# Optimization experiments

Measured on AMD Instinct MI355X. Metric: run time of the kernel, lower is better.

Reference implementation:

```python
import jax, jax.numpy as jnp
import numpy as np
from jax.scipy.linalg import block_diag

N_STATE, N_INPUT, HORIZON = 32, 16, 64


def setup_inputs() -> dict:
    key = jax.random.key(0)
    kA, kB, kC, kx = jax.random.split(key, 4)
    n_all = N_STATE + N_INPUT
    A = jax.random.normal(kA, (N_STATE, N_STATE), dtype=jnp.float32)
    B = jax.random.normal(kB, (N_STATE, N_INPUT), dtype=jnp.float32)
    Craw = jax.random.normal(kC, (HORIZON, n_all, n_all), dtype=jnp.float32)
    # symmetric positive-definite stage costs -> nonsingular KKT system
    C = jnp.einsum('tij,tkj->tik', Craw, Craw) / jnp.sqrt(jnp.float32(n_all)) \
        + jnp.eye(n_all, dtype=jnp.float32)
    x0 = jax.random.normal(kx, (N_STATE,), dtype=jnp.float32)
    return {"A": A, "B": B, "C": C, "T": HORIZON, "x0": x0}


def reference(A, B, C, T, x0):
    n_state = A.shape[0]
    n_input = B.shape[1]
    n_all = n_state + n_input
    dt = A.dtype

    # cost_mat: block-diagonal [n_all*T, n_all*T]
    cost_mat = block_diag(*C)

    # dynamics: [n_state*T, n_all*T]
    AB = jnp.concatenate((A, B), axis=1)              # [n_state, n_all]
    AB_blk = block_diag(*([AB] * (T - 1)))            # [(T-1)*n_state, (T-1)*n_all]
    dynamics = jnp.zeros((n_state * T, n_all * T), dtype=dt)
    dynamics = dynamics.at[:n_state, :n_state].set(jnp.eye(n_state, dtype=dt))
    dynamics = dynamics.at[n_state:n_state + (T - 1) * n_state,
                           :(T - 1) * n_all].set(AB_blk)
    # -I coupling entries: row n_state*t + i, col n_all*t + i, t=1..T-1
    t = jnp.arange(1, T)
    rows = (n_state * t)[:, None] + jnp.arange(n_state)[None, :]
    cols = (n_all * t)[:, None] + jnp.arange(n_state)[None, :]
    dynamics = dynamics.at[rows, cols].set(jnp.asarray(-1.0, dt))

    zero_mat = jnp.zeros((n_state * T, n_state * T), dtype=dt)
    full_mat = jnp.block([[cost_mat, dynamics.T],
                          [dynamics, zero_mat]])      # [(n_all+n_state)*T]^2

    # rhs: zeros except x0 at the start of the dynamics block
    sol = jnp.zeros(n_all * T + n_state * T, dtype=dt)
    sol = sol.at[n_all * T: n_all * T + n_state].set(x0)

    tau_mu = jnp.linalg.solve(full_mat, sol[:, None])[:, 0]
    tau_star = tau_mu[:n_all * T]
    mu_star = tau_mu[n_all * T:]
    return tau_star, mu_star
```

## Files before the change

### kernel.cpp

```cpp
#include <hip/hip_runtime.h>


namespace {

constexpr int NS  = 32;
constexpr int NI  = 16;
constexpr int NA  = 48;
constexpr int TT  = 64;
constexpr int NTH = 256;
constexpr int NBLK = 64;

using ull = unsigned long long;

__device__ __forceinline__ void fma4(float4& a, float s, const float4& b) {
  a.x += s * b.x; a.y += s * b.y; a.z += s * b.z; a.w += s * b.w;
}
__device__ __forceinline__ void fms4(float4& a, float s, const float4& b) {
  a.x -= s * b.x; a.y -= s * b.y; a.z -= s * b.z; a.w -= s * b.w;
}
__device__ __forceinline__ float dot4(const float4& a, const float4& b) {
  return a.x * b.x + a.y * b.y + a.z * b.z + a.w * b.w;
}
__device__ __forceinline__ float rdlane(float v, int l) {
  return __int_as_float(__builtin_amdgcn_readlane(__float_as_int(v), l));
}

__device__ __forceinline__ ull ald(const ull* p) {
  return __hip_atomic_load(p, __ATOMIC_RELAXED, __HIP_MEMORY_SCOPE_AGENT);
}
__device__ __forceinline__ void ast(ull* p, ull v) {
  __hip_atomic_store(p, v, __ATOMIC_RELAXED, __HIP_MEMORY_SCOPE_AGENT);
}
__device__ __forceinline__ float aldf(const float* p) {
  return __uint_as_float(__hip_atomic_load((const unsigned*)p,
      __ATOMIC_RELAXED, __HIP_MEMORY_SCOPE_AGENT));
}
__device__ __forceinline__ void astf(float* p, float v) {
  __hip_atomic_store((unsigned*)p, __float_as_uint(v),
      __ATOMIC_RELAXED, __HIP_MEMORY_SCOPE_AGENT);
}
__device__ __forceinline__ ull pack2(float x, float y) {
  return (ull)__float_as_uint(x) | ((ull)__float_as_uint(y) << 32);
}
__device__ __forceinline__ float2 unpack2(ull v) {
  return make_float2(__uint_as_float((unsigned)v),
                     __uint_as_float((unsigned)(v >> 32)));
}
__device__ __forceinline__ float4 ald4(const ull* p) {
  ull lo = ald(p), hi = ald(p + 1);
  float2 a = unpack2(lo), b = unpack2(hi);
  return make_float4(a.x, a.y, b.x, b.y);
}
__device__ __forceinline__ void ast4(ull* p, const float4& v) {
  ast(p, pack2(v.x, v.y)); ast(p + 1, pack2(v.z, v.w));
}

__device__ __forceinline__ unsigned fld(const unsigned* f) {
  return __hip_atomic_load(f, __ATOMIC_RELAXED, __HIP_MEMORY_SCOPE_AGENT);
}
__device__ __forceinline__ void fst(unsigned* f) {
  __hip_atomic_store(f, 1u, __ATOMIC_RELAXED, __HIP_MEMORY_SCOPE_AGENT);
}
__device__ __forceinline__ void waitf(const unsigned* f) {
  if (threadIdx.x == 0)
    while (fld(f) == 0) __builtin_amdgcn_s_sleep(1);
  __syncthreads();
}
__device__ __forceinline__ void setf(unsigned* f) {
  asm volatile("s_waitcnt vmcnt(0)" ::: "memory");
  __syncthreads();
  if (threadIdx.x == 0) fst(f);
}

template<int K>
__device__ __forceinline__ void tile_outer(const float* Acol0, int lda,
                                           const float* Bcol0, int ldb,
                                           float4 acc[4]) {
  #pragma unroll
  for (int m = 0; m < K; ++m) {
    const float4 va = *(const float4*)(Acol0 + m * lda);
    const float4 vb = *(const float4*)(Bcol0 + m * ldb);
    fma4(acc[0], va.x, vb); fma4(acc[1], va.y, vb);
    fma4(acc[2], va.z, vb); fma4(acc[3], va.w, vb);
  }
}

template<int KQ>
__device__ __forceinline__ void tile_dot(const float* Arow0, int lda,
                                         const float* Brow0, int ldb,
                                         float acc[4][4]) {
  #pragma unroll
  for (int q = 0; q < KQ; ++q) {
    float4 va[4], vb[4];
    #pragma unroll
    for (int r = 0; r < 4; ++r) va[r] = *(const float4*)(Arow0 + r * lda + 4 * q);
    #pragma unroll
    for (int c = 0; c < 4; ++c) vb[c] = *(const float4*)(Brow0 + c * ldb + 4 * q);
    #pragma unroll
    for (int r = 0; r < 4; ++r)
      #pragma unroll
      for (int c = 0; c < 4; ++c) acc[r][c] += dot4(va[r], vb[c]);
  }
}

__device__ __forceinline__ float step_dot(const float4 m[8], float x) {
  float a0 = 0.f, a1 = 0.f, a2 = 0.f, a3 = 0.f;
  #pragma unroll
  for (int q = 0; q < 8; ++q) {
    a0 += rdlane(x, 4 * q + 0) * m[q].x;
    a1 += rdlane(x, 4 * q + 1) * m[q].y;
    a2 += rdlane(x, 4 * q + 2) * m[q].z;
    a3 += rdlane(x, 4 * q + 3) * m[q].w;
  }
  return (a0 + a1) + (a2 + a3);
}

__device__ __forceinline__ int nlev(int rm) {
  return (rm == TT - 1) ? 0 : (32 - __clz(TT - 1 - rm));
}

__global__ __launch_bounds__(NTH, 1) void lqr_all(
    const float* __restrict__ A, const float* __restrict__ Bm,
    const float* __restrict__ C, const float* __restrict__ x0,
    float* __restrict__ out,
    float* __restrict__ Sb0, float* __restrict__ Sb1,
    float* __restrict__ Mall, float* __restrict__ xs,
    unsigned* __restrict__ flg) {
  __shared__ float sC [NA][NA];
  __shared__ float sAB[NS][NA];
  __shared__ float sRiST[NS][NI];
  __shared__ float sBRi [NS][NI];
  __shared__ float sAi[NS][NS], sCi[NS][NS], sJi[NS][NS];
  __shared__ float sAj[NS][NS], sCj[NS][NS], sJj[NS][NS], sAjT[NS][NS];
  __shared__ float sV[NS][NS], sU[NS][NS];
  __shared__ float sY1[NS][NS], sY2[NS][NS], sW[NS][NS];
  __shared__ float sX[NS][NS], sZm[NS][NS];
  __shared__ float sG[NS][NA], sFu[NI][NA], sK[NI][NS], sK2[NI][NS];
  __shared__ float sXt0[NS], sXt1[NS];

  const int t = blockIdx.x, tid = threadIdx.x, lane = tid & 63, wid = tid >> 6;
  unsigned* wr = flg;
  unsigned* rd = flg + 448;
  unsigned* mf = flg + 832;
  unsigned* xf = flg + 896;

  {
    const float* Ct = C + (size_t)t * NA * NA;
    for (int e = tid; e < NA * NA; e += NTH) sC[e / NA][e % NA] = Ct[e];
    for (int e = tid; e < NS * NA; e += NTH) {
      int i = e / NA, j = e % NA;
      sAB[i][j] = (j < NS) ? A[i * NS + j] : Bm[i * NI + (j - NS)];
    }
    __syncthreads();
    if (wid < 2 && lane < 48) {
      const int c = lane;
      float f[NI];
      if (c < NI) {
        #pragma unroll
        for (int i = 0; i < NI; ++i) f[i] = sC[NS + i][NS + c];
      } else {
        const int a = c - NI;
        if (wid == 0) {
          #pragma unroll
          for (int i = 0; i < NI; ++i) f[i] = sC[a][NS + i];
        } else {
          #pragma unroll
          for (int i = 0; i < NI; ++i) f[i] = sAB[a][NS + i];
        }
      }
      #pragma unroll
      for (int k = 0; k < NI; ++k) {
        float mi[NI];
        #pragma unroll
        for (int i = 0; i < NI; ++i) mi[i] = rdlane(f[i], k);
        const float inv = 1.0f / mi[k];
        f[k] *= inv;
        #pragma unroll
        for (int i = 0; i < NI; ++i) if (i != k) f[i] -= mi[i] * f[k];
      }
      if (c >= NI) {
        const int a = c - NI;
        float* D = (wid == 0) ? &sRiST[a][0] : &sBRi[a][0];
        #pragma unroll
        for (int i = 0; i < NI; ++i) D[i] = f[i];
      }
    }
    __syncthreads();
    ull* outA = (ull*)(Sb0 + (size_t)t * 3072);
    ull* outC = outA + 512;
    ull* outJ = outA + 1024;
    if (tid < 64) {
      const int a = tid >> 3, b = tid & 7;
      float acc[4][4];
      #pragma unroll
      for (int r = 0; r < 4; ++r)
        #pragma unroll
        for (int c = 0; c < 4; ++c) acc[r][c] = 0.f;
      tile_dot<4>(&sRiST[4 * a][0], NI, &sC[4 * b][NS], NA, acc);
      #pragma unroll
      for (int r = 0; r < 4; ++r) {
        const float4 q4 = *(const float4*)&sC[4 * a + r][4 * b];
        const float4 v = make_float4(q4.x - acc[r][0], q4.y - acc[r][1],
                                     q4.z - acc[r][2], q4.w - acc[r][3]);
        *(float4*)&sJi[4 * a + r][4 * b] = v;
        ast4(outJ + ((4 * a + r) * NS + 4 * b) / 2, v);
      }
    } else if (tid < 128) {
      const int q = tid - 64, a = q >> 3, b = q & 7;
      float acc[4][4];
      #pragma unroll
      for (int r = 0; r < 4; ++r)
        #pragma unroll
        for (int c = 0; c < 4; ++c) acc[r][c] = 0.f;
      tile_dot<4>(&sBRi[4 * a][0], NI, &sC[4 * b][NS], NA, acc);
      #pragma unroll
      for (int r = 0; r < 4; ++r) {
        const float4 a4 = *(const float4*)&sAB[4 * a + r][4 * b];
        const float4 v = make_float4(a4.x - acc[r][0], a4.y - acc[r][1],
                                     a4.z - acc[r][2], a4.w - acc[r][3]);
        *(float4*)&sAi[4 * a + r][4 * b] = v;
        ast4(outA + ((4 * a + r) * NS + 4 * b) / 2, v);
      }
    } else if (tid < 192) {
      const int q = tid - 128, a = q >> 3, b = q & 7;
      float acc[4][4];
      #pragma unroll
      for (int r = 0; r < 4; ++r)
        #pragma unroll
        for (int c = 0; c < 4; ++c) acc[r][c] = 0.f;
      tile_dot<4>(&sBRi[4 * a][0], NI, &sAB[4 * b][NS], NA, acc);
      #pragma unroll
      for (int r = 0; r < 4; ++r) {
        const float4 v = make_float4(acc[r][0], acc[r][1], acc[r][2], acc[r][3]);
        *(float4*)&sCi[4 * a + r][4 * b] = v;
        ast4(outC + ((4 * a + r) * NS + 4 * b) / 2, v);
      }
    }
  }
  setf(&wr[0 * 64 + t]);

  auto combine = [&]() {
    #pragma unroll
    for (int r = 0; r < 4; ++r) {
      const int e = tid + 256 * r, i = e >> 5, j = e & 31;
      sAjT[j][i] = sAj[i][j];
    }
    if (tid < 64) {
      const int a = tid >> 3, b = tid & 7;
      float4 acc[4] = {make_float4(0,0,0,0), make_float4(0,0,0,0),
                       make_float4(0,0,0,0), make_float4(0,0,0,0)};
      tile_outer<NS>(&sCi[0][4 * a], NS, &sJj[0][4 * b], NS, acc);
      if (a == b) { acc[0].x += 1.f; acc[1].y += 1.f; acc[2].z += 1.f; acc[3].w += 1.f; }
      #pragma unroll
      for (int r = 0; r < 4; ++r) *(float4*)&sX[4 * a + r][4 * b] = acc[r];
    }
    __syncthreads();
    if (wid < 2) {
      const int c = lane;
      float f[NS];
      if (c < NS) {
        #pragma unroll
        for (int i = 0; i < NS; ++i) f[i] = sX[i][c];
      } else if (wid == 0) {
        #pragma unroll
        for (int i = 0; i < NS; ++i) f[i] = sAi[i][c - NS];
      } else {
        #pragma unroll
        for (int i = 0; i < NS; ++i) f[i] = sCi[i][c - NS];
      }
      #pragma unroll
      for (int k = 0; k < NS; ++k) {
        float mi[NS];
        #pragma unroll
        for (int i = 0; i < NS; ++i) mi[i] = rdlane(f[i], k);
        const float inv = 1.0f / mi[k];
        f[k] *= inv;
        #pragma unroll
        for (int i = 0; i < NS; ++i) if (i != k) f[i] -= mi[i] * f[k];
      }
      if (c >= NS) {
        const int col = c - NS;
        if (wid == 0) {
          #pragma unroll
          for (int i = 0; i < NS; ++i) sV[i][col] = f[i];
        } else {
          #pragma unroll
          for (int i = 0; i < NS; ++i) sU[i][col] = f[i];
        }
      }
    }
    __syncthreads();
    if (tid < 192) {
      const int grp = tid >> 6, q = tid & 63, a = q >> 3, b = q & 7;
      float4 acc[4] = {make_float4(0,0,0,0), make_float4(0,0,0,0),
                       make_float4(0,0,0,0), make_float4(0,0,0,0)};
      if (grp == 0) {
        tile_outer<NS>(&sJj[0][4 * a], NS, &sV[0][4 * b], NS, acc);
        #pragma unroll
        for (int r = 0; r < 4; ++r) *(float4*)&sW[4 * a + r][4 * b] = acc[r];
      } else if (grp == 1) {
        tile_outer<NS>(&sAjT[0][4 * a], NS, &sV[0][4 * b], NS, acc);
        #pragma unroll
        for (int r = 0; r < 4; ++r) *(float4*)&sX[4 * a + r][4 * b] = acc[r];
      } else {
        tile_outer<NS>(&sAjT[0][4 * a], NS, &sU[0][4 * b], NS, acc);
        #pragma unroll
        for (int r = 0; r < 4; ++r) *(float4*)&sZm[4 * a + r][4 * b] = acc[r];
      }
    }
    __syncthreads();
    if (tid < 64) {
      const int a = tid >> 3, b = tid & 7;
      float4 acc[4] = {make_float4(0,0,0,0), make_float4(0,0,0,0),
                       make_float4(0,0,0,0), make_float4(0,0,0,0)};
      tile_outer<NS>(&sAi[0][4 * a], NS, &sW[0][4 * b], NS, acc);
      #pragma unroll
      for (int r = 0; r < 4; ++r) {
        const float4 j4 = *(const float4*)&sJi[4 * a + r][4 * b];
        acc[r].x += j4.x; acc[r].y += j4.y; acc[r].z += j4.z; acc[r].w += j4.w;
        *(float4*)&sY1[4 * a + r][4 * b] = acc[r];
      }
    } else if (tid < 128) {
      const int q = tid - 64, a = q >> 3, b = q & 7;
      float acc[4][4];
      #pragma unroll
      for (int r = 0; r < 4; ++r)
        #pragma unroll
        for (int c = 0; c < 4; ++c) acc[r][c] = 0.f;
      tile_dot<8>(&sZm[4 * a][0], NS, &sAj[4 * b][0], NS, acc);
      #pragma unroll
      for (int r = 0; r < 4; ++r) {
        const float4 c4 = *(const float4*)&sCj[4 * a + r][4 * b];
        *(float4*)&sY2[4 * a + r][4 * b] =
            make_float4(acc[r][0] + c4.x, acc[r][1] + c4.y,
                        acc[r][2] + c4.z, acc[r][3] + c4.w);
      }
    }
    __syncthreads();
    ((ull*)sAi)[tid] = ((const ull*)sX)[tid];
    ((ull*)sAi)[tid + 256] = ((const ull*)sX)[tid + 256];
    ((ull*)sCi)[tid] = ((const ull*)sY2)[tid];
    ((ull*)sCi)[tid + 256] = ((const ull*)sY2)[tid + 256];
    ((ull*)sJi)[tid] = ((const ull*)sY1)[tid];
    ((ull*)sJi)[tid + 256] = ((const ull*)sY1)[tid + 256];
    __syncthreads();
  };

  for (int l = 0; l < 6; ++l) {
    const int off = 1 << l;
    const int rm = t + off;
    if (rm < TT) {
      const int nlv = nlev(rm);
      const int v = (l < nlv) ? l : nlv;
      const float* Sin = (v & 1) ? Sb1 : Sb0;
      float* Sout = ((l + 1) & 1) ? Sb1 : Sb0;
      ull* Eo = (ull*)(Sout + (size_t)t * 3072);
      waitf(&wr[v * 64 + rm]);
      const ull* Ej = (const ull*)(Sin + (size_t)rm * 3072);
      {
        ull r0 = ald(Ej + tid),        r1 = ald(Ej + 256 + tid);
        ull r2 = ald(Ej + 512 + tid),  r3 = ald(Ej + 768 + tid);
        ull r4 = ald(Ej + 1024 + tid), r5 = ald(Ej + 1280 + tid);
        ((ull*)sAj)[tid] = r0; ((ull*)sAj)[tid + 256] = r1;
        ((ull*)sCj)[tid] = r2; ((ull*)sCj)[tid + 256] = r3;
        ((ull*)sJj)[tid] = r4; ((ull*)sJj)[tid + 256] = r5;
      }
      __syncthreads();
      if (v == l && tid == 0) fst(&rd[l * 64 + rm]);
      combine();
      if (l >= 1 && t >= (off >> 1)) waitf(&rd[(l - 1) * 64 + t]);
      ast(Eo + tid,        ((const ull*)sAi)[tid]);
      ast(Eo + 256 + tid,  ((const ull*)sAi)[tid + 256]);
      ast(Eo + 512 + tid,  ((const ull*)sCi)[tid]);
      ast(Eo + 768 + tid,  ((const ull*)sCi)[tid + 256]);
      ast(Eo + 1024 + tid, ((const ull*)sJi)[tid]);
      ast(Eo + 1280 + tid, ((const ull*)sJi)[tid + 256]);
      setf(&wr[(l + 1) * 64 + t]);
    }
  }

  auto kmat = [&](int tau, bool hasP, float (*Pm)[NS], float (*Kd)[NS], bool wM) {
    const int ui = tid / 12, uk = tid - 12 * ui;
    float4 cr0 = make_float4(0,0,0,0), cr1 = make_float4(0,0,0,0);
    float4 cr2 = make_float4(0,0,0,0), cr3 = make_float4(0,0,0,0);
    if (tid < 48) {
      const float* Ct = C + (size_t)tau * NA * NA;
      cr0 = *(const float4*)&Ct[(NS + 4 * ui + 0) * NA + 4 * uk];
      cr1 = *(const float4*)&Ct[(NS + 4 * ui + 1) * NA + 4 * uk];
      cr2 = *(const float4*)&Ct[(NS + 4 * ui + 2) * NA + 4 * uk];
      cr3 = *(const float4*)&Ct[(NS + 4 * ui + 3) * NA + 4 * uk];
    }
    if (hasP) {
      if (tid < 96) {
        const int gi = tid / 12, gk = tid - 12 * gi;
        float4 acc[4] = {make_float4(0,0,0,0), make_float4(0,0,0,0),
                         make_float4(0,0,0,0), make_float4(0,0,0,0)};
        tile_outer<NS>(&Pm[0][4 * gi], NS, &sAB[0][4 * gk], NA, acc);
        #pragma unroll
        for (int r = 0; r < 4; ++r) *(float4*)&sG[4 * gi + r][4 * gk] = acc[r];
      }
    } else {
      for (int e = tid; e < NS * NA; e += NTH) sG[e / NA][e % NA] = 0.f;
    }
    __syncthreads();
    if (tid < 48) {
      float4 acc[4] = {cr0, cr1, cr2, cr3};
      tile_outer<NS>(&sAB[0][NS + 4 * ui], NA, &sG[0][4 * uk], NA, acc);
      #pragma unroll
      for (int r = 0; r < 4; ++r) *(float4*)&sFu[4 * ui + r][4 * uk] = acc[r];
    }
    __syncthreads();
    if (wid == 0) {
      const int col = (lane < 16) ? (NS + lane) : (lane - 16);
      float f[NI];
      #pragma unroll
      for (int i = 0; i < NI; ++i) f[i] = sFu[i][col];
      #pragma unroll
      for (int k = 0; k < NI; ++k) {
        float mi[NI];
        #pragma unroll
        for (int i = 0; i < NI; ++i) mi[i] = rdlane(f[i], k);
        const float inv = 1.0f / mi[k];
        f[k] *= inv;
        #pragma unroll
        for (int i = 0; i < NI; ++i) if (i != k) f[i] -= mi[i] * f[k];
      }
      if (lane >= 16 && lane < 48) {
        const int b = lane - 16;
        #pragma unroll
        for (int i = 0; i < NI; ++i) Kd[i][b] = f[i];
      }
    }
    __syncthreads();
    if (wM && tid < 64) {
      const int ma = tid >> 3, mb = tid & 7;
      float4 a0 = *(const float4*)&sAB[4 * ma + 0][4 * mb];
      float4 a1 = *(const float4*)&sAB[4 * ma + 1][4 * mb];
      float4 a2 = *(const float4*)&sAB[4 * ma + 2][4 * mb];
      float4 a3 = *(const float4*)&sAB[4 * ma + 3][4 * mb];
      #pragma unroll
      for (int q = 0; q < 4; ++q) {
        const float4 vf0 = *(const float4*)&sAB[4 * ma + 0][NS + 4 * q];
        const float4 vf1 = *(const float4*)&sAB[4 * ma + 1][NS + 4 * q];
        const float4 vf2 = *(const float4*)&sAB[4 * ma + 2][NS + 4 * q];
        const float4 vf3 = *(const float4*)&sAB[4 * ma + 3][NS + 4 * q];
        #pragma unroll
        for (int d = 0; d < 4; ++d) {
          const float4 vkk = *(const float4*)&Kd[4 * q + d][4 * mb];
          const float s0 = (d == 0) ? vf0.x : (d == 1) ? vf0.y : (d == 2) ? vf0.z : vf0.w;
          const float s1 = (d == 0) ? vf1.x : (d == 1) ? vf1.y : (d == 2) ? vf1.z : vf1.w;
          const float s2 = (d == 0) ? vf2.x : (d == 1) ? vf2.y : (d == 2) ? vf2.z : vf2.w;
          const float s3 = (d == 0) ? vf3.x : (d == 1) ? vf3.y : (d == 2) ? vf3.z : vf3.w;
          fms4(a0, s0, vkk); fms4(a1, s1, vkk); fms4(a2, s2, vkk); fms4(a3, s3, vkk);
        }
      }
      ull* Mt = (ull*)(Mall + (size_t)tau * NS * NS);
      ast4(Mt + (4 * ma + 0) * 16 + 2 * mb, a0);
      ast4(Mt + (4 * ma + 1) * 16 + 2 * mb, a1);
      ast4(Mt + (4 * ma + 2) * 16 + 2 * mb, a2);
      ast4(Mt + (4 * ma + 3) * 16 + 2 * mb, a3);
    }
    __syncthreads();
  };

  if (t >= 1) kmat(t - 1, true, sJi, sK, true);
  if (t == TT - 1) kmat(TT - 1, false, nullptr, sK2, false);
  setf(&mf[t]);

  if (t == 0) {
    if (tid < NBLK) {
      while (fld(&mf[tid]) == 0) __builtin_amdgcn_s_sleep(1);
    }
    __syncthreads();
    if (wid == 0) {
      const int i = lane;
      if (i < NS) {
        const ull* Mg = (const ull*)Mall;
        float4 mA[8], mB[8];
        float x = x0[i];
        out[i] = x; astf(&xs[i], x);
        #pragma unroll
        for (int q = 0; q < 8; ++q) mA[q] = ald4(Mg + 0 * 512 + i * 16 + 2 * q);
        #pragma unroll
        for (int q = 0; q < 8; ++q) mB[q] = ald4(Mg + 1 * 512 + i * 16 + 2 * q);
        for (int s = 0; s < TT - 1; s += 2) {
          x = step_dot(mA, x);
          out[(s + 1) * NA + i] = x; astf(&xs[(s + 1) * NS + i], x);
          if (s + 2 < TT - 1) {
            #pragma unroll
            for (int q = 0; q < 8; ++q) mA[q] = ald4(Mg + (s + 2) * 512 + i * 16 + 2 * q);
          }
          if (s + 1 < TT - 1) {
            x = step_dot(mB, x);
            out[(s + 2) * NA + i] = x; astf(&xs[(s + 2) * NS + i], x);
            if (s + 3 < TT - 1) {
              #pragma unroll
              for (int q = 0; q < 8; ++q) mB[q] = ald4(Mg + (s + 3) * 512 + i * 16 + 2 * q);
            }
          }
        }
      }
    }
    setf(xf);
  }
  waitf(xf);

  {
    if (tid < NS) sXt0[tid] = aldf(&xs[(size_t)t * NS + tid]);
    else if (tid >= 64 && tid < 64 + NS && t >= 1)
      sXt1[tid - 64] = aldf(&xs[(size_t)(t - 1) * NS + (tid - 64)]);
    __syncthreads();
    if (t >= 1 && tid < NI) {
      const float4* Kr = (const float4*)&sK[tid][0];
      const float4* xr = (const float4*)sXt1;
      float acc = 0.f;
      #pragma unroll
      for (int q = 0; q < 8; ++q) acc += dot4(Kr[q], xr[q]);
      out[(t - 1) * NA + NS + tid] = -acc;
    } else if (tid >= NI && tid < NI + NS) {
      const int i = tid - NI;
      const float4* Pr = (const float4*)&sJi[i][0];
      const float4* xr = (const float4*)sXt0;
      float acc = 0.f;
      #pragma unroll
      for (int q = 0; q < 8; ++q) acc += dot4(Pr[q], xr[q]);
      out[NA * TT + t * NS + i] = (t == 0) ? -acc : acc;
    } else if (t == TT - 1 && tid >= 192 && tid < 192 + NI) {
      const int i = tid - 192;
      const float4* Kr = (const float4*)&sK2[i][0];
      const float4* xr = (const float4*)sXt0;
      float acc = 0.f;
      #pragma unroll
      for (int q = 0; q < 8; ++q) acc += dot4(Kr[q], xr[q]);
      out[(TT - 1) * NA + NS + i] = -acc;
    }
  }
}

}

extern "C" void kernel_launch(void* const* d_in, const int* in_sizes, int n_in,
                              void* d_out, int out_size, void* d_ws, size_t ws_size,
                              hipStream_t stream) {
  const float* A  = (const float*)d_in[0];
  const float* Bm = (const float*)d_in[1];
  const float* C  = (const float*)d_in[2];
  const float* x0 = (const float*)d_in[4];
  float* out = (float*)d_out;

  float* Sb0 = (float*)d_ws;
  float* Sb1 = Sb0 + (size_t)TT * 3072;
  float* Mall = Sb1 + (size_t)TT * 3072;
  float* xs   = Mall + (size_t)TT * NS * NS;
  unsigned* flg = (unsigned*)(xs + (size_t)TT * NS);

  hipMemsetAsync(flg, 0, 4096, stream);
  hipLaunchKernelGGL(lqr_all, dim3(NBLK), dim3(NTH), 0, stream,
                     A, Bm, C, x0, out, Sb0, Sb1, Mall, xs, flg);
}
```

Measured before the change: 143.3 us.

## Compute forward state rollout redundantly per block instead of broadcasting from block 0

Each block now waits on all M flags and runs the forward recurrence itself up to its own stage t, keeping x_t and x_{t-1} in shared memory. This removes the xs global buffer, block 0's serial broadcast and the xf flag wait, trading a cross-block handoff for redundant serial work (up to 63 steps in the last block). It also remaps blockIdx to t with a bit-swizzle, likely to spread stages across XCDs, and pads sAjT rows to 36 to reduce LDS bank conflicts.

New measurement: 126.6 us. 11.6% less time.

```diff
diff --git a/kernel.cpp b/kernel.cpp
--- a/kernel.cpp
+++ b/kernel.cpp
@@ -30,14 +30,6 @@
 }
 __device__ __forceinline__ void ast(ull* p, ull v) {
   __hip_atomic_store(p, v, __ATOMIC_RELAXED, __HIP_MEMORY_SCOPE_AGENT);
-}
-__device__ __forceinline__ float aldf(const float* p) {
-  return __uint_as_float(__hip_atomic_load((const unsigned*)p,
-      __ATOMIC_RELAXED, __HIP_MEMORY_SCOPE_AGENT));
-}
-__device__ __forceinline__ void astf(float* p, float v) {
-  __hip_atomic_store((unsigned*)p, __float_as_uint(v),
-      __ATOMIC_RELAXED, __HIP_MEMORY_SCOPE_AGENT);
 }
 __device__ __forceinline__ ull pack2(float x, float y) {
   return (ull)__float_as_uint(x) | ((ull)__float_as_uint(y) << 32);
@@ -124,25 +116,25 @@
     const float* __restrict__ C, const float* __restrict__ x0,
     float* __restrict__ out,
     float* __restrict__ Sb0, float* __restrict__ Sb1,
-    float* __restrict__ Mall, float* __restrict__ xs,
-    unsigned* __restrict__ flg) {
+    float* __restrict__ Mall, unsigned* __restrict__ flg) {
   __shared__ float sC [NA][NA];
   __shared__ float sAB[NS][NA];
   __shared__ float sRiST[NS][NI];
   __shared__ float sBRi [NS][NI];
   __shared__ float sAi[NS][NS], sCi[NS][NS], sJi[NS][NS];
-  __shared__ float sAj[NS][NS], sCj[NS][NS], sJj[NS][NS], sAjT[NS][NS];
+  __shared__ float sAj[NS][NS], sCj[NS][NS], sJj[NS][NS];
+  __shared__ float sAjT[NS][36];
   __shared__ float sV[NS][NS], sU[NS][NS];
   __shared__ float sY1[NS][NS], sY2[NS][NS], sW[NS][NS];
   __shared__ float sX[NS][NS], sZm[NS][NS];
   __shared__ float sG[NS][NA], sFu[NI][NA], sK[NI][NS], sK2[NI][NS];
   __shared__ float sXt0[NS], sXt1[NS];
 
-  const int t = blockIdx.x, tid = threadIdx.x, lane = tid & 63, wid = tid >> 6;
+  const int t = ((blockIdx.x & 7) << 3) | (blockIdx.x >> 3);
+  const int tid = threadIdx.x, lane = tid & 63, wid = tid >> 6;
   unsigned* wr = flg;
   unsigned* rd = flg + 448;
   unsigned* mf = flg + 832;
-  unsigned* xf = flg + 896;
 
   {
     const float* Ct = C + (size_t)t * NA * NA;
@@ -299,11 +291,11 @@
         #pragma unroll
         for (int r = 0; r < 4; ++r) *(float4*)&sW[4 * a + r][4 * b] = acc[r];
       } else if (grp == 1) {
-        tile_outer<NS>(&sAjT[0][4 * a], NS, &sV[0][4 * b], NS, acc);
+        tile_outer<NS>(&sAjT[0][4 * a], 36, &sV[0][4 * b], NS, acc);
         #pragma unroll
         for (int r = 0; r < 4; ++r) *(float4*)&sX[4 * a + r][4 * b] = acc[r];
       } else {
-        tile_outer<NS>(&sAjT[0][4 * a], NS, &sU[0][4 * b], NS, acc);
+        tile_outer<NS>(&sAjT[0][4 * a], 36, &sU[0][4 * b], NS, acc);
         #pragma unroll
         for (int r = 0; r < 4; ++r) *(float4*)&sZm[4 * a + r][4 * b] = acc[r];
       }
@@ -467,7 +459,7 @@
   if (t == TT - 1) kmat(TT - 1, false, nullptr, sK2, false);
   setf(&mf[t]);
 
-  if (t == 0) {
+  {
     if (tid < NBLK) {
       while (fld(&mf[tid]) == 0) __builtin_amdgcn_s_sleep(1);
     }
@@ -478,38 +470,41 @@
         const ull* Mg = (const ull*)Mall;
         float4 mA[8], mB[8];
         float x = x0[i];
-        out[i] = x; astf(&xs[i], x);
-        #pragma unroll
-        for (int q = 0; q < 8; ++q) mA[q] = ald4(Mg + 0 * 512 + i * 16 + 2 * q);
-        #pragma unroll
-        for (int q = 0; q < 8; ++q) mB[q] = ald4(Mg + 1 * 512 + i * 16 + 2 * q);
-        for (int s = 0; s < TT - 1; s += 2) {
+        if (t == 1) sXt1[i] = x;
+        if (t >= 1) {
+          #pragma unroll
+          for (int q = 0; q < 8; ++q) mA[q] = ald4(Mg + 0 * 512 + i * 16 + 2 * q);
+        }
+        if (t >= 2) {
+          #pragma unroll
+          for (int q = 0; q < 8; ++q) mB[q] = ald4(Mg + 1 * 512 + i * 16 + 2 * q);
+        }
+        for (int s = 0; s < t; s += 2) {
           x = step_dot(mA, x);
-          out[(s + 1) * NA + i] = x; astf(&xs[(s + 1) * NS + i], x);
-          if (s + 2 < TT - 1) {
+          if (s + 1 == t - 1) sXt1[i] = x;
+          if (s + 2 < t) {
             #pragma unroll
-            for (int q = 0; q < 8; ++q) mA[q] = ald4(Mg + (s + 2) * 512 + i * 16 + 2 * q);
+            for (int q = 0; q < 8; ++q)
+              mA[q] = ald4(Mg + (s + 2) * 512 + i * 16 + 2 * q);
           }
-          if (s + 1 < TT - 1) {
+          if (s + 1 < t) {
             x = step_dot(mB, x);
-            out[(s + 2) * NA + i] = x; astf(&xs[(s + 2) * NS + i], x);
-            if (s + 3 < TT - 1) {
+            if (s + 2 == t - 1) sXt1[i] = x;
+            if (s + 3 < t) {
               #pragma unroll
-              for (int q = 0; q < 8; ++q) mB[q] = ald4(Mg + (s + 3) * 512 + i * 16 + 2 * q);
+              for (int q = 0; q < 8; ++q)
+                mB[q] = ald4(Mg + (s + 3) * 512 + i * 16 + 2 * q);
             }
           }
         }
-      }
-    }
-    setf(xf);
-  }
-  waitf(xf);
+        sXt0[i] = x;
+        out[t * NA + i] = x;
+      }
+    }
+    __syncthreads();
+  }
 
   {
-    if (tid < NS) sXt0[tid] = aldf(&xs[(size_t)t * NS + tid]);
-    else if (tid >= 64 && tid < 64 + NS && t >= 1)
-      sXt1[tid - 64] = aldf(&xs[(size_t)(t - 1) * NS + (tid - 64)]);
-    __syncthreads();
     if (t >= 1 && tid < NI) {
       const float4* Kr = (const float4*)&sK[tid][0];
       const float4* xr = (const float4*)sXt1;
@@ -551,10 +546,9 @@
   float* Sb0 = (float*)d_ws;
   float* Sb1 = Sb0 + (size_t)TT * 3072;
   float* Mall = Sb1 + (size_t)TT * 3072;
-  float* xs   = Mall + (size_t)TT * NS * NS;
-  unsigned* flg = (unsigned*)(xs + (size_t)TT * NS);
+  unsigned* flg = (unsigned*)(Mall + (size_t)TT * NS * NS);
 
   hipMemsetAsync(flg, 0, 4096, stream);
   hipLaunchKernelGGL(lqr_all, dim3(NBLK), dim3(NTH), 0, stream,
-                     A, Bm, C, x0, out, Sb0, Sb1, Mall, xs, flg);
-}
+                     A, Bm, C, x0, out, Sb0, Sb1, Mall, flg);
+}
```
